# Optimization experiments

Hardware: AMD Instinct MI355X
Metric: run time of the kernel (lower is better)

## Reference

```python
import jax, jax.numpy as jnp
import numpy as np

ROPE_DIM = 64
ROPE_THETA = 10000.0
SLIDING_WINDOW = 1024
_K_MASK = jnp.finfo(jnp.bfloat16).min


def _pos_embeddings(positions, head_dim, rope_theta):
    # positions: [B, T] -> sin, cos: [B, T, head_dim]
    fraction = jnp.arange(0, head_dim, 2, dtype=jnp.float32) / head_dim
    inv_freq = 1.0 / (rope_theta ** fraction)
    sinusoid = jnp.einsum('BT,k->BTk', positions.astype(jnp.float32), inv_freq,
                          precision=jax.lax.Precision.HIGHEST)
    sin = jnp.sin(sinusoid); cos = jnp.cos(sinusoid)
    return jnp.concatenate([sin, sin], -1), jnp.concatenate([cos, cos], -1)


def _rotate_half(x):
    x1, x2 = x[..., :x.shape[-1] // 2], x[..., x.shape[-1] // 2:]
    return jnp.concatenate([-x2, x1], -1)


def _apply_rope_partial(x, sin, cos, rope_dim):
    x_rope, x_nope = x[..., :rope_dim], x[..., rope_dim:]
    sin = sin[:, :, None, :]; cos = cos[:, :, None, :]
    x_rope = x_rope * cos + _rotate_half(x_rope) * sin
    return jnp.concatenate([x_rope, x_nope], -1).astype(x.dtype)


def setup_inputs() -> dict:
    key = jax.random.key(0)
    ks = jax.random.split(key, 6)
    B, T, D = 2, 2048, 2048
    N, K, H, Hv = 16, 4, 128, 128
    S = 2048  # cache size
    sc = 0.02
    return {
        'x': jax.random.normal(ks[0], (B, T, D), jnp.float32),
        'wq': jax.random.normal(ks[1], (D, N, H), jnp.float32) * sc,
        'wk': jax.random.normal(ks[2], (D, K, H), jnp.float32) * sc,
        'wv': jax.random.normal(ks[3], (D, K, Hv), jnp.float32) * sc,
        'wo': jax.random.normal(ks[4], (N, Hv, D), jnp.float32) * sc,
        'sink_bias': jnp.zeros((N,), jnp.float32),
        'k_cache': jnp.zeros((B, S, K, H), jnp.float32),
        'v_cache': jnp.zeros((B, S, K, Hv), jnp.float32),
        'segment_ids': jnp.ones((B, T), jnp.int32),
        'cur_ind': 0,
        'start_ind': -jnp.ones((B,), jnp.int32),
    }


def reference(x, wq, wk, wv, wo, sink_bias, k_cache, v_cache,
              segment_ids, cur_ind, start_ind):
    B, T, D = x.shape
    N, H = wq.shape[1], wq.shape[2]
    K, Hv = wk.shape[1], wv.shape[2]
    n_rep = N // K
    scaling = H ** -0.5
    cur_ind = jnp.asarray(cur_ind, jnp.int32)

    q = jnp.einsum('BTD,DNH->BTNH', x, wq)
    k = jnp.einsum('BSD,DKH->BSKH', x, wk)
    v = jnp.einsum('BSD,DKV->BSKV', x, wv)

    # left pads / positions from segment ids
    left_pads = jnp.sum(jnp.cumsum(segment_ids != 0, axis=-1) == 0, -1).astype(jnp.int32)
    start = jnp.where(start_ind < 0, left_pads, start_ind)
    pos = jax.vmap(lambda row: jnp.where(row != 0,
                                         jnp.arange(T, dtype=jnp.int32) - jnp.argmax(row).astype(jnp.int32),
                                         2 ** 30))(segment_ids) + cur_ind
    sin, cos = _pos_embeddings(pos, ROPE_DIM, ROPE_THETA)
    q = _apply_rope_partial(q, sin, cos, ROPE_DIM)
    k = _apply_rope_partial(k, sin, cos, ROPE_DIM)

    # KV cache append
    kc = jax.lax.dynamic_update_slice(k_cache, k, (0, cur_ind, 0, 0))
    vc = jax.lax.dynamic_update_slice(v_cache, v, (0, cur_ind, 0, 0))
    S = kc.shape[1]

    # GQA repeat
    kr = jnp.repeat(kc[:, :, :, None, :], n_rep, axis=3).reshape(B, S, N, H)
    vr = jnp.repeat(vc[:, :, :, None, :], n_rep, axis=3).reshape(B, S, N, Hv)

    logits = jnp.einsum('BTNH,BSNH->BTNS', q, kr) * scaling

    q_pos = cur_ind + jnp.arange(T, dtype=jnp.int32)[None, :] - start[:, None]
    ts = jnp.arange(S, dtype=jnp.int32)
    kv_seg = (ts[None, :] >= start[:, None]) & (ts[None, :] < cur_ind + T)
    k_pos = ts[None, :] - start[:, None]
    causal = k_pos[:, None, :] <= q_pos[:, :, None]
    seg_mask = kv_seg[:, None, :] == segment_ids[:, :, None]
    window = k_pos[:, None, :] >= q_pos[:, :, None] - (SLIDING_WINDOW - 1)
    final_mask = causal & seg_mask & window  # [B, T, S]
    logits = jnp.where(final_mask[:, :, None, :], logits, _K_MASK)

    # attention sink bias: extra softmax slot per head
    sink = jnp.broadcast_to(sink_bias[None, None, :, None], (B, T, N, 1))
    logits = jnp.concatenate([logits, sink], axis=-1)
    weights = jax.nn.softmax(logits.astype(jnp.float32), axis=-1).astype(logits.dtype)
    weights = weights[..., :-1]

    attn = jnp.einsum('BTNS,BSNV->BTNV', weights, vr)
    return jnp.einsum('BTNV,NVD->BTD', attn, wo)
```

## Files before the change

### kernel.cpp

```cpp
#include <hip/hip_runtime.h>
#include <hip/hip_bf16.h>
#include <stdint.h>

#define BB 2
#define TT 2048
#define DD 2048
#define NHQ 16
#define KH 4
#define HD 128
#define SS 2048
#define WINDOW 1024
#define M2FIX 12.0f
#define QSC_LOG2E 0.12751751f
#define LOG2E 1.4426950408889634f
#define NLOG2F 0.4152410118609203f

typedef __attribute__((ext_vector_type(8))) short bf16x8;
typedef __attribute__((ext_vector_type(4))) float f32x4;
typedef __attribute__((ext_vector_type(16))) float f32x16;

#define MFMA16(a, b, c) __builtin_amdgcn_mfma_f32_16x16x32_bf16(a, b, c, 0, 0, 0)
#define MFMA32(a, b, c) __builtin_amdgcn_mfma_f32_32x32x16_bf16(a, b, c, 0, 0, 0)

__device__ __forceinline__ ushort f2bf(float f) {
  uint32_t u = __float_as_uint(f);
  u += 0x7FFF + ((u >> 16) & 1);
  return (ushort)(u >> 16);
}
__device__ __forceinline__ ushort f2bf_trunc(float f) {
  return (ushort)(__float_as_uint(f) >> 16);
}
__device__ __forceinline__ float bf2f(ushort h) {
  return __uint_as_float(((uint32_t)h) << 16);
}

__device__ __forceinline__ void async_copy16(const ushort* g, ushort* l) {
  __builtin_amdgcn_global_load_lds(
      (const __attribute__((address_space(1))) uint32_t*)g,
      (__attribute__((address_space(3))) uint32_t*)l, 16, 0, 0);
}

__device__ __forceinline__ void tr_tile(const float* __restrict__ in,
                                        ushort* __restrict__ out,
                                        int C, int ldo, int cx, int cy) {
  __shared__ float tile[32][33];
  int tx = threadIdx.x & 31, ty = threadIdx.x >> 5;
  int r0 = cy * 32, c0 = cx * 32;
#pragma unroll
  for (int k = 0; k < 4; k++)
    tile[ty + k * 8][tx] = in[(size_t)(r0 + ty + k * 8) * C + c0 + tx];
  __syncthreads();
#pragma unroll
  for (int k = 0; k < 4; k++)
    out[(size_t)(c0 + ty + k * 8) * ldo + r0 + tx] = f2bf(tile[tx][ty + k * 8]);
}

__global__ void prep_fused(const float* __restrict__ x, const float* __restrict__ wq,
                           const float* __restrict__ wk, const float* __restrict__ wv,
                           const float* __restrict__ wo, const int* __restrict__ seg,
                           const int* __restrict__ start_ind, ushort* __restrict__ xb,
                           ushort* __restrict__ WcatT, ushort* __restrict__ WoT,
                           int* __restrict__ meta) {
  int bz = blockIdx.x;
  int tid = threadIdx.x;
  if (bz < 2) {
    __shared__ int red[256];
    int b = bz;
    int first = TT;
    for (int t = tid; t < TT; t += 256)
      if (seg[b * TT + t] != 0) first = min(first, t);
    red[tid] = first;
    __syncthreads();
    for (int s = 128; s > 0; s >>= 1) {
      if (tid < s) red[tid] = min(red[tid], red[tid + s]);
      __syncthreads();
    }
    if (tid == 0) {
      int fi = red[0];
      int st = start_ind[b] < 0 ? fi : start_ind[b];
      meta[b * 2 + 0] = st;
      meta[b * 2 + 1] = (fi >= TT) ? 0 : fi;
    }
    return;
  }
  bz -= 2;
  if (bz < 2048) {
#pragma unroll
    for (int p = 0; p < 4; p++) {
      int i = bz * 1024 + p * 256 + tid;
      float4 v = ((const float4*)x)[i];
      ushort4 o;
      o.x = f2bf(v.x); o.y = f2bf(v.y); o.z = f2bf(v.z); o.w = f2bf(v.w);
      ((ushort4*)xb)[i] = o;
    }
    return;
  }
  bz -= 2048;
  if (bz < 4096) { tr_tile(wq, WcatT, 2048, 2048, bz & 63, bz >> 6); return; }
  bz -= 4096;
  if (bz < 1024) { tr_tile(wk, WcatT + (size_t)2048 * 2048, 512, 2048, bz & 15, bz >> 4); return; }
  bz -= 1024;
  if (bz < 1024) { tr_tile(wv, WcatT + (size_t)2560 * 2048, 512, 2048, bz & 15, bz >> 4); return; }
  bz -= 1024;
  tr_tile(wo, WoT, 2048, 2048, bz & 63, bz >> 6);
}

__global__ __launch_bounds__(256) void gemm_qkv(const ushort* __restrict__ A,
                                                const ushort* __restrict__ Bt,
                                                const int* __restrict__ seg,
                                                const int* __restrict__ cur_p,
                                                const int* __restrict__ meta,
                                                ushort* __restrict__ qa,
                                                ushort* __restrict__ ka,
                                                ushort* __restrict__ vat) {
  const int K = DD;
  __shared__ ushort SH[16640];
  ushort* As = SH;
  ushort* Bs = SH + 8192;
  float* posf_s = (float*)(SH + 16384);
  int tid = threadIdx.x;
  int lane = tid & 63, wave = tid >> 6;
  int wr = wave >> 1, wc = wave & 1;
  int orig = blockIdx.y * 24 + blockIdx.x;
  int wid = (orig & 7) * 96 + (orig >> 3);
  int by = wid / 24, bx = wid - by * 24;
  int row0 = by * 128, col0 = bx * 128;
  int l31 = lane & 31, khalf = lane >> 5, lx8 = l31 & 7;
  int cur = cur_p[0];

  if (tid < 128) {
    int m = row0 + tid;
    int bb = m >> 11, t = m & 2047;
    int segv = seg[m];
    int first = meta[bb * 2 + 1];
    posf_s[tid] = (segv != 0) ? (float)(t - first + cur) : 1073741824.0f;
  }

  f32x16 acc[2][2];
#pragma unroll
  for (int i = 0; i < 2; i++)
#pragma unroll
    for (int j = 0; j < 2; j++)
#pragma unroll
      for (int e = 0; e < 16; e++) acc[i][j][e] = 0.f;

  int srow = tid >> 3, scol = tid & 7;
  int ssw = (scol ^ (srow & 7)) * 8;
  const ushort* Ag = A  + (size_t)(row0 + srow) * K + ssw;
  const ushort* Bg = Bt + (size_t)(col0 + srow) * K + ssw;
  ushort* AsD = As + tid * 8;
  ushort* BsD = Bs + tid * 8;

  for (int kc = 0; kc < K; kc += 64) {
    __syncthreads();
#pragma unroll
    for (int p = 0; p < 4; p++)
      async_copy16(Ag + kc + (size_t)(p * 32) * K, AsD + p * 2048);
#pragma unroll
    for (int p = 0; p < 4; p++)
      async_copy16(Bg + kc + (size_t)(p * 32) * K, BsD + p * 2048);
    __syncthreads();
#pragma unroll
    for (int ks = 0; ks < 4; ks++) {
      bf16x8 af[2], bfm[2];
      int ch = (ks * 2 + khalf) ^ lx8;
#pragma unroll
      for (int i = 0; i < 2; i++)
        af[i] = *(const bf16x8*)(As + (wr * 64 + i * 32 + l31) * 64 + ch * 8);
#pragma unroll
      for (int j = 0; j < 2; j++)
        bfm[j] = *(const bf16x8*)(Bs + (wc * 64 + j * 32 + l31) * 64 + ch * 8);
#pragma unroll
      for (int i = 0; i < 2; i++)
#pragma unroll
        for (int j = 0; j < 2; j++)
          acc[i][j] = MFMA32(af[i], bfm[j], acc[i][j]);
    }
  }

  int cb0 = col0 + wc * 64;
  int region = (cb0 < 2048) ? 0 : (cb0 < 2560 ? 1 : 2);

  if (region <= 1) {
    bool ropehalf = ((cb0 & 64) == 0);
    int hbase = cb0 & 64;
    float invf = exp2f(-NLOG2F * (float)l31);
#pragma unroll
    for (int i = 0; i < 2; i++) {
#pragma unroll
      for (int reg = 0; reg < 16; reg++) {
        int rloc = wr * 64 + i * 32 + (reg & 3) + 8 * (reg >> 2) + 4 * khalf;
        int m = row0 + rloc;
        int b = m >> 11, t = m & 2047;
        float v0 = acc[i][0][reg], v1 = acc[i][1][reg];
        if (ropehalf) {
          float posf = posf_s[rloc];
          float sn, cs;
          __sincosf(posf * invf, &sn, &cs);
          float n0 = v0 * cs - v1 * sn;
          v1 = v1 * cs + v0 * sn;
          v0 = n0;
        }
        if (region == 0) {
          int head = cb0 >> 7;
          size_t base = ((size_t)(b * NHQ + head) * TT + t) * HD + hbase;
          qa[base + l31]      = f2bf(v0 * QSC_LOG2E);
          qa[base + 32 + l31] = f2bf(v1 * QSC_LOG2E);
        } else {
          int head = (cb0 - 2048) >> 7;
          size_t rowbase = ((size_t)(b * KH + head) * SS + t) * HD;
          int sw = t & 7;
          int c0x = hbase + l31, c1x = hbase + 32 + l31;
          ka[rowbase + ((((c0x >> 3) ^ sw) << 3) | (c0x & 7))] = f2bf(v0);
          ka[rowbase + ((((c1x >> 3) ^ sw) << 3) | (c1x & 7))] = f2bf(v1);
        }
      }
    }
  } else {
    __syncthreads();
    ushort* TB = SH;
    int hbase = wc * 64;
#pragma unroll
    for (int i = 0; i < 2; i++)
#pragma unroll
      for (int reg = 0; reg < 16; reg++) {
        int rloc = wr * 64 + i * 32 + (reg & 3) + 8 * (reg >> 2) + 4 * khalf;
        int h0 = hbase + l31, h1 = hbase + 32 + l31;
        TB[h0 * 128 + (rloc ^ ((h0 & 15) << 3))] = f2bf(acc[i][0][reg]);
        TB[h1 * 128 + (rloc ^ ((h1 & 15) << 3))] = f2bf(acc[i][1][reg]);
      }
    __syncthreads();
    int headv = (col0 - 2560) >> 7;
    int bv = row0 >> 11;
    ushort* vout = vat + (size_t)(bv * KH + headv) * HD * SS + (row0 & 2047);
#pragma unroll
    for (int pass = 0; pass < 8; pass++) {
      int idx = pass * 256 + tid;
      int h = idx >> 4, cc = idx & 15;
      int s64 = cc >> 3, c = cc & 7;
      bf16x8 vd = *(const bf16x8*)(TB + h * 128 + (s64 ^ ((h >> 3) & 1)) * 64 + c * 8);
      *(bf16x8*)(vout + (size_t)h * SS + s64 * 64 + c * 8) = vd;
    }
  }
}

template <int OUT_F32>
__global__ __launch_bounds__(256) void gemm_bt(const ushort* __restrict__ A,
                                               const ushort* __restrict__ Bt,
                                               void* __restrict__ Cout,
                                               int M, int N, int K) {
  __shared__ ushort As[128 * 64];
  __shared__ ushort Bs[128 * 64];
  int tid = threadIdx.x;
  int lane = tid & 63, wave = tid >> 6;
  int wr = wave >> 1, wc = wave & 1;
  int orig = blockIdx.y * gridDim.x + blockIdx.x;
  int nwg = gridDim.x * gridDim.y;
  int cpx = nwg >> 3;
  int wid = (orig & 7) * cpx + (orig >> 3);
  int by = wid / gridDim.x, bx = wid - by * gridDim.x;
  int row0 = by * 128, col0 = bx * 128;
  int l31 = lane & 31, khalf = lane >> 5, lx8 = l31 & 7;

  f32x16 acc[2][2];
#pragma unroll
  for (int i = 0; i < 2; i++)
#pragma unroll
    for (int j = 0; j < 2; j++)
#pragma unroll
      for (int e = 0; e < 16; e++) acc[i][j][e] = 0.f;

  int srow = tid >> 3, scol = tid & 7;
  int ssw = (scol ^ (srow & 7)) * 8;
  const ushort* Ag = A  + (size_t)(row0 + srow) * K + ssw;
  const ushort* Bg = Bt + (size_t)(col0 + srow) * K + ssw;
  ushort* AsD = As + tid * 8;
  ushort* BsD = Bs + tid * 8;

  for (int kc = 0; kc < K; kc += 64) {
    __syncthreads();
#pragma unroll
    for (int p = 0; p < 4; p++)
      async_copy16(Ag + kc + (size_t)(p * 32) * K, AsD + p * 2048);
#pragma unroll
    for (int p = 0; p < 4; p++)
      async_copy16(Bg + kc + (size_t)(p * 32) * K, BsD + p * 2048);
    __syncthreads();
#pragma unroll
    for (int ks = 0; ks < 4; ks++) {
      bf16x8 af[2], bfm[2];
      int ch = (ks * 2 + khalf) ^ lx8;
#pragma unroll
      for (int i = 0; i < 2; i++)
        af[i] = *(const bf16x8*)(As + (wr * 64 + i * 32 + l31) * 64 + ch * 8);
#pragma unroll
      for (int j = 0; j < 2; j++)
        bfm[j] = *(const bf16x8*)(Bs + (wc * 64 + j * 32 + l31) * 64 + ch * 8);
#pragma unroll
      for (int i = 0; i < 2; i++)
#pragma unroll
        for (int j = 0; j < 2; j++)
          acc[i][j] = MFMA32(af[i], bfm[j], acc[i][j]);
    }
  }

#pragma unroll
  for (int i = 0; i < 2; i++)
#pragma unroll
    for (int reg = 0; reg < 16; reg++) {
      int r = row0 + wr * 64 + i * 32 + (reg & 3) + 8 * (reg >> 2) + 4 * khalf;
#pragma unroll
      for (int j = 0; j < 2; j++) {
        int c = col0 + wc * 64 + j * 32 + l31;
        float v = acc[i][j][reg];
        if (OUT_F32)
          ((float*)Cout)[(size_t)r * N + c] = v;
        else
          ((ushort*)Cout)[(size_t)r * N + c] = f2bf(v);
      }
    }
}

__global__ __launch_bounds__(256) void flash_attn(
    const ushort* __restrict__ qa, const ushort* __restrict__ ka,
    const ushort* __restrict__ vat, const float* __restrict__ sink_bias,
    const int* __restrict__ seg, const int* __restrict__ cur_p,
    const int* __restrict__ meta, ushort* __restrict__ Obuf) {
  __shared__ ushort Ks[64 * 128];
  __shared__ ushort VT[128 * 64];
  __shared__ ushort Ps[4 * 2048];

  int bxx = blockIdx.x;
  int kb = bxx & 3, b = (bxx >> 2) & 1;
  int jr = bxx >> 3;
  int j32 = (jr & 1) ? (63 - (jr >> 1)) : (jr >> 1);
  int t0 = j32 * 32;
  int cur = cur_p[0];
  int start = meta[b * 2];

  int tid = threadIdx.x, lane = tid & 63, w = tid >> 6;
  int n = kb * 4 + w;
  int lcol = lane & 15, quad = lane >> 4, lx = lcol & 7;

  const ushort* qbase = qa + (size_t)(b * NHQ + n) * TT * HD;
  const ushort* kbase = ka + (size_t)(b * KH + kb) * SS * HD;
  const ushort* vtb   = vat + (size_t)(b * KH + kb) * HD * SS;

  bf16x8 qf[2][4];
  int segq[2][4], trow[2][4], seg1[2];
#pragma unroll
  for (int g = 0; g < 2; g++) {
    const ushort* qrow = qbase + (size_t)(t0 + g * 16 + lcol) * HD + quad * 8;
#pragma unroll
    for (int c = 0; c < 4; c++) qf[g][c] = *(const bf16x8*)(qrow + c * 32);
#pragma unroll
    for (int r = 0; r < 4; r++) {
      trow[g][r] = t0 + g * 16 + quad * 4 + r;
      segq[g][r] = seg[b * TT + trow[g][r]];
    }
    seg1[g] = __all(segq[g][0] == 1 && segq[g][1] == 1 &&
                    segq[g][2] == 1 && segq[g][3] == 1);
  }

  f32x4 oacc[2][8], lacc[2];
#pragma unroll
  for (int g = 0; g < 2; g++) {
#pragma unroll
    for (int ob = 0; ob < 8; ob++) { f32x4 z = {0.f, 0.f, 0.f, 0.f}; oacc[g][ob] = z; }
    f32x4 z = {0.f, 0.f, 0.f, 0.f}; lacc[g] = z;
  }

  bf16x8 ones;
#pragma unroll
  for (int e = 0; e < 8; e++) ones[e] = (short)0x3F80;

  ushort* KsD = Ks + tid * 8;
  ushort* VTD = VT + tid * 8;
  const ushort* KgT = kbase + tid * 8;
  const ushort* VgT = vtb + (size_t)(tid >> 3) * SS + (tid & 7) * 8;

  int lo = cur + t0 - (WINDOW - 1); if (lo < 0) lo = 0;
  int hi = cur + t0 + 31;           if (hi > SS - 1) hi = SS - 1;
  int ktlo = lo >> 6, kthi = hi >> 6;

  for (int kt = ktlo; kt <= kthi; kt++) {
    int ks0 = kt * 64;
    __syncthreads();
#pragma unroll
    for (int p = 0; p < 4; p++)
      async_copy16(KgT + (size_t)ks0 * 128 + p * 2048, KsD + p * 2048);
#pragma unroll
    for (int p = 0; p < 4; p++)
      async_copy16(VgT + ks0 + (size_t)p * 32 * SS, VTD + p * 2048);
    __syncthreads();

#pragma unroll
    for (int g = 0; g < 2; g++) {
      int t0g = t0 + g * 16;
      bool active = (ks0 <= cur + t0g + 15) && (ks0 + 63 >= cur + t0g - (WINDOW - 1));
      if (!active) continue;

      ushort* PsG = Ps + w * 2048 + g * 1024;
      f32x4 sacc[4];
#pragma unroll
      for (int cb = 0; cb < 4; cb++) { f32x4 z = {0.f, 0.f, 0.f, 0.f}; sacc[cb] = z; }
#pragma unroll
      for (int c = 0; c < 4; c++) {
#pragma unroll
        for (int cb = 0; cb < 4; cb++) {
          bf16x8 kf = *(const bf16x8*)(Ks + (cb * 16 + lcol) * 128 +
                                       (((c * 4 + quad) ^ lx)) * 8);
          sacc[cb] = MFMA16(qf[g][c], kf, sacc[cb]);
        }
      }

      bool fast = seg1[g] && (ks0 >= start) && (ks0 + 63 <= cur + t0g) &&
                  (ks0 >= cur + t0g + 15 - (WINDOW - 1));
      if (fast) {
#pragma unroll
        for (int r = 0; r < 4; r++) {
          int row = quad * 4 + r;
#pragma unroll
          for (int cb = 0; cb < 4; cb++) {
            float p = exp2f(sacc[cb][r] - M2FIX);
            PsG[row * 64 + (((cb * 2 + (lcol >> 3)) ^ (row & 7)) * 8) + lx] = f2bf_trunc(p);
          }
        }
      } else {
        int sidx[4], kvseg[4];
#pragma unroll
        for (int cb = 0; cb < 4; cb++) {
          sidx[cb] = ks0 + cb * 16 + lcol;
          kvseg[cb] = (sidx[cb] >= start && sidx[cb] < cur + TT) ? 1 : 0;
        }
#pragma unroll
        for (int r = 0; r < 4; r++) {
          int row = quad * 4 + r;
          int qp = (segq[g][r] != 0) ? (cur + trow[g][r]) : (1 << 29);
#pragma unroll
          for (int cb = 0; cb < 4; cb++) {
            bool ok = (sidx[cb] <= qp) && (sidx[cb] >= qp - (WINDOW - 1)) &&
                      (kvseg[cb] == segq[g][r]);
            float p = ok ? exp2f(sacc[cb][r] - M2FIX) : 0.f;
            PsG[row * 64 + (((cb * 2 + (lcol >> 3)) ^ (row & 7)) * 8) + lx] = f2bf_trunc(p);
          }
        }
      }

#pragma unroll
      for (int c2 = 0; c2 < 2; c2++) {
        bf16x8 pf = *(const bf16x8*)(PsG + lcol * 64 + (((c2 * 4 + quad) ^ lx)) * 8);
#pragma unroll
        for (int ob = 0; ob < 8; ob++) {
          bf16x8 vf = *(const bf16x8*)(VT + (ob * 16 + lcol) * 64 +
                                       (((c2 * 4 + quad) ^ lx)) * 8);
          oacc[g][ob] = MFMA16(pf, vf, oacc[g][ob]);
        }
        lacc[g] = MFMA16(pf, ones, lacc[g]);
      }
    }
  }

  float sb = sink_bias[n];
#pragma unroll
  for (int g = 0; g < 2; g++) {
#pragma unroll
    for (int r = 0; r < 4; r++) {
      float l = lacc[g][r] + exp2f(sb * LOG2E - M2FIX);
      float inv = 1.f / l;
      int t = trow[g][r];
      size_t base = ((size_t)(b * TT + t)) * (NHQ * HD) + n * HD;
#pragma unroll
      for (int ob = 0; ob < 8; ob++)
        Obuf[base + ob * 16 + lcol] = f2bf(oacc[g][ob][r] * inv);
    }
  }
}

extern "C" void kernel_launch(void* const* d_in, const int* in_sizes, int n_in,
                              void* d_out, int out_size, void* d_ws, size_t ws_size,
                              hipStream_t stream) {
  const float* x  = (const float*)d_in[0];
  const float* wq = (const float*)d_in[1];
  const float* wk = (const float*)d_in[2];
  const float* wv = (const float*)d_in[3];
  const float* wo = (const float*)d_in[4];
  const float* sink = (const float*)d_in[5];
  const int* seg = (const int*)d_in[8];
  const int* cur = (const int*)d_in[9];
  const int* start_ind = (const int*)d_in[10];

  char* ws = (char*)d_ws;
  ushort* xb    = (ushort*)(ws + 0);
  ushort* WcatT = (ushort*)(ws + 16777216);
  ushort* WoT   = (ushort*)(ws + 29360128);
  ushort* qa    = (ushort*)(ws + 37748736);
  ushort* ka    = (ushort*)(ws + 54525952);
  ushort* vat   = (ushort*)(ws + 62914560);
  ushort* Obuf  = (ushort*)(ws + 67108864);
  int*    meta  = (int*)(ws + 83886080);

  prep_fused<<<12290, 256, 0, stream>>>(x, wq, wk, wv, wo, seg, start_ind,
                                        xb, WcatT, WoT, meta);
  gemm_qkv<<<dim3(24, 32), 256, 0, stream>>>(xb, WcatT, seg, cur, meta, qa, ka, vat);
  flash_attn<<<512, 256, 0, stream>>>(qa, ka, vat, sink, seg, cur, meta, Obuf);
  gemm_bt<1><<<dim3(16, 32), 256, 0, stream>>>(Obuf, WoT, d_out, 4096, 2048, 2048);
}
```

Baseline: 333.7 us.

## Restructure flash attention to one head per block and vectorize transpose tiles

The attention kernel moves from blocks of four heads sharing a KV group over 32 query rows to blocks of two waves handling one head over 64 query rows, each wave covering 32 rows. The QK and PV MFMAs for both 16-row groups are interleaved so each K and V fragment read from LDS feeds two MFMAs, and the grid gets a new query-tile order meant to balance load. In exchange, each K/V tile load now serves one head instead of four, which increases KV traffic, and inactive groups write explicit zeros to Ps. The prep transpose tile is also changed to use float4 loads and ushort4 stores.

```diff
diff --git a/kernel.cpp b/kernel.cpp
--- a/kernel.cpp
+++ b/kernel.cpp
@@ -43,16 +43,20 @@
 __device__ __forceinline__ void tr_tile(const float* __restrict__ in,
                                         ushort* __restrict__ out,
                                         int C, int ldo, int cx, int cy) {
-  __shared__ float tile[32][33];
-  int tx = threadIdx.x & 31, ty = threadIdx.x >> 5;
+  __shared__ float tile[32][36];
+  int t = threadIdx.x;
   int r0 = cy * 32, c0 = cx * 32;
-#pragma unroll
-  for (int k = 0; k < 4; k++)
-    tile[ty + k * 8][tx] = in[(size_t)(r0 + ty + k * 8) * C + c0 + tx];
+  int row = t >> 3, c4 = (t & 7) * 4;
+  float4 v = *(const float4*)&in[(size_t)(r0 + row) * C + c0 + c4];
+  *(float4*)&tile[row][c4] = v;
   __syncthreads();
-#pragma unroll
-  for (int k = 0; k < 4; k++)
-    out[(size_t)(c0 + ty + k * 8) * ldo + r0 + tx] = f2bf(tile[tx][ty + k * 8]);
+  int oc = t >> 3, or4 = (t & 7) * 4;
+  ushort4 o;
+  o.x = f2bf(tile[or4 + 0][oc]);
+  o.y = f2bf(tile[or4 + 1][oc]);
+  o.z = f2bf(tile[or4 + 2][oc]);
+  o.w = f2bf(tile[or4 + 3][oc]);
+  *(ushort4*)&out[(size_t)(c0 + oc) * ldo + r0 + or4] = o;
 }
 
 __global__ void prep_fused(const float* __restrict__ x, const float* __restrict__ wq,
@@ -321,26 +325,28 @@
     }
 }
 
-__global__ __launch_bounds__(256) void flash_attn(
+__global__ __launch_bounds__(128) void flash_attn(
     const ushort* __restrict__ qa, const ushort* __restrict__ ka,
     const ushort* __restrict__ vat, const float* __restrict__ sink_bias,
     const int* __restrict__ seg, const int* __restrict__ cur_p,
     const int* __restrict__ meta, ushort* __restrict__ Obuf) {
   __shared__ ushort Ks[64 * 128];
   __shared__ ushort VT[128 * 64];
-  __shared__ ushort Ps[4 * 2048];
-
-  int bxx = blockIdx.x;
-  int kb = bxx & 3, b = (bxx >> 2) & 1;
-  int jr = bxx >> 3;
-  int j32 = (jr & 1) ? (63 - (jr >> 1)) : (jr >> 1);
-  int t0 = j32 * 32;
+  __shared__ ushort Ps[4096];
+
+  int bx = blockIdx.x;
+  int u = bx & 255, v = bx >> 8;
+  int combo = u & 31, j5 = u >> 5;
+  int b = combo >> 4, n = combo & 15;
+  int qt = (v == 0) ? j5 : (v == 1) ? (15 - j5) : (v == 2) ? (16 + j5) : (31 - j5);
+  int kb = n >> 2;
+  int t0 = qt * 64;
   int cur = cur_p[0];
   int start = meta[b * 2];
 
   int tid = threadIdx.x, lane = tid & 63, w = tid >> 6;
-  int n = kb * 4 + w;
   int lcol = lane & 15, quad = lane >> 4, lx = lcol & 7;
+  int tw = t0 + w * 32;
 
   const ushort* qbase = qa + (size_t)(b * NHQ + n) * TT * HD;
   const ushort* kbase = ka + (size_t)(b * KH + kb) * SS * HD;
@@ -350,12 +356,12 @@
   int segq[2][4], trow[2][4], seg1[2];
 #pragma unroll
   for (int g = 0; g < 2; g++) {
-    const ushort* qrow = qbase + (size_t)(t0 + g * 16 + lcol) * HD + quad * 8;
+    const ushort* qrow = qbase + (size_t)(tw + g * 16 + lcol) * HD + quad * 8;
 #pragma unroll
     for (int c = 0; c < 4; c++) qf[g][c] = *(const bf16x8*)(qrow + c * 32);
 #pragma unroll
     for (int r = 0; r < 4; r++) {
-      trow[g][r] = t0 + g * 16 + quad * 4 + r;
+      trow[g][r] = tw + g * 16 + quad * 4 + r;
       segq[g][r] = seg[b * TT + trow[g][r]];
     }
     seg1[g] = __all(segq[g][0] == 1 && segq[g][1] == 1 &&
@@ -370,9 +376,9 @@
     f32x4 z = {0.f, 0.f, 0.f, 0.f}; lacc[g] = z;
   }
 
-  bf16x8 ones;
-#pragma unroll
-  for (int e = 0; e < 8; e++) ones[e] = (short)0x3F80;
+  bf16x8 ones, zeros;
+#pragma unroll
+  for (int e = 0; e < 8; e++) { ones[e] = (short)0x3F80; zeros[e] = 0; }
 
   ushort* KsD = Ks + tid * 8;
   ushort* VTD = VT + tid * 8;
@@ -380,40 +386,52 @@
   const ushort* VgT = vtb + (size_t)(tid >> 3) * SS + (tid & 7) * 8;
 
   int lo = cur + t0 - (WINDOW - 1); if (lo < 0) lo = 0;
-  int hi = cur + t0 + 31;           if (hi > SS - 1) hi = SS - 1;
+  int hi = cur + t0 + 63;           if (hi > SS - 1) hi = SS - 1;
   int ktlo = lo >> 6, kthi = hi >> 6;
+
+  ushort* PsW = Ps + w * 2048;
 
   for (int kt = ktlo; kt <= kthi; kt++) {
     int ks0 = kt * 64;
     __syncthreads();
 #pragma unroll
-    for (int p = 0; p < 4; p++)
-      async_copy16(KgT + (size_t)ks0 * 128 + p * 2048, KsD + p * 2048);
-#pragma unroll
-    for (int p = 0; p < 4; p++)
-      async_copy16(VgT + ks0 + (size_t)p * 32 * SS, VTD + p * 2048);
-    __syncthreads();
+    for (int p = 0; p < 8; p++)
+      async_copy16(KgT + (size_t)ks0 * 128 + p * 1024, KsD + p * 1024);
+#pragma unroll
+    for (int p = 0; p < 8; p++)
+      async_copy16(VgT + ks0 + (size_t)p * 16 * SS, VTD + p * 1024);
+    __syncthreads();
+
+    int act0 = (ks0 <= cur + tw + 15)      && (ks0 + 63 >= cur + tw - (WINDOW - 1));
+    int act1 = (ks0 <= cur + tw + 16 + 15) && (ks0 + 63 >= cur + tw + 16 - (WINDOW - 1));
+    if (!(act0 | act1)) continue;
+
+    f32x4 sacc[2][4];
+#pragma unroll
+    for (int g = 0; g < 2; g++)
+#pragma unroll
+      for (int cb = 0; cb < 4; cb++) { f32x4 z = {0.f, 0.f, 0.f, 0.f}; sacc[g][cb] = z; }
+#pragma unroll
+    for (int c = 0; c < 4; c++) {
+#pragma unroll
+      for (int cb = 0; cb < 4; cb++) {
+        bf16x8 kf = *(const bf16x8*)(Ks + (cb * 16 + lcol) * 128 +
+                                     (((c * 4 + quad) ^ lx)) * 8);
+        sacc[0][cb] = MFMA16(qf[0][c], kf, sacc[0][cb]);
+        sacc[1][cb] = MFMA16(qf[1][c], kf, sacc[1][cb]);
+      }
+    }
 
 #pragma unroll
     for (int g = 0; g < 2; g++) {
-      int t0g = t0 + g * 16;
-      bool active = (ks0 <= cur + t0g + 15) && (ks0 + 63 >= cur + t0g - (WINDOW - 1));
-      if (!active) continue;
-
-      ushort* PsG = Ps + w * 2048 + g * 1024;
-      f32x4 sacc[4];
-#pragma unroll
-      for (int cb = 0; cb < 4; cb++) { f32x4 z = {0.f, 0.f, 0.f, 0.f}; sacc[cb] = z; }
-#pragma unroll
-      for (int c = 0; c < 4; c++) {
-#pragma unroll
-        for (int cb = 0; cb < 4; cb++) {
-          bf16x8 kf = *(const bf16x8*)(Ks + (cb * 16 + lcol) * 128 +
-                                       (((c * 4 + quad) ^ lx)) * 8);
-          sacc[cb] = MFMA16(qf[g][c], kf, sacc[cb]);
-        }
-      }
-
+      ushort* PsG = PsW + g * 1024;
+      int act = g ? act1 : act0;
+      if (!act) {
+        *(bf16x8*)(PsG + lane * 16) = zeros;
+        *(bf16x8*)(PsG + lane * 16 + 8) = zeros;
+        continue;
+      }
+      int t0g = tw + g * 16;
       bool fast = seg1[g] && (ks0 >= start) && (ks0 + 63 <= cur + t0g) &&
                   (ks0 >= cur + t0g + 15 - (WINDOW - 1));
       if (fast) {
@@ -422,7 +440,7 @@
           int row = quad * 4 + r;
 #pragma unroll
           for (int cb = 0; cb < 4; cb++) {
-            float p = exp2f(sacc[cb][r] - M2FIX);
+            float p = exp2f(sacc[g][cb][r] - M2FIX);
             PsG[row * 64 + (((cb * 2 + (lcol >> 3)) ^ (row & 7)) * 8) + lx] = f2bf_trunc(p);
           }
         }
@@ -441,23 +459,26 @@
           for (int cb = 0; cb < 4; cb++) {
             bool ok = (sidx[cb] <= qp) && (sidx[cb] >= qp - (WINDOW - 1)) &&
                       (kvseg[cb] == segq[g][r]);
-            float p = ok ? exp2f(sacc[cb][r] - M2FIX) : 0.f;
+            float p = ok ? exp2f(sacc[g][cb][r] - M2FIX) : 0.f;
             PsG[row * 64 + (((cb * 2 + (lcol >> 3)) ^ (row & 7)) * 8) + lx] = f2bf_trunc(p);
           }
         }
       }
-
-#pragma unroll
-      for (int c2 = 0; c2 < 2; c2++) {
-        bf16x8 pf = *(const bf16x8*)(PsG + lcol * 64 + (((c2 * 4 + quad) ^ lx)) * 8);
-#pragma unroll
-        for (int ob = 0; ob < 8; ob++) {
-          bf16x8 vf = *(const bf16x8*)(VT + (ob * 16 + lcol) * 64 +
-                                       (((c2 * 4 + quad) ^ lx)) * 8);
-          oacc[g][ob] = MFMA16(pf, vf, oacc[g][ob]);
-        }
-        lacc[g] = MFMA16(pf, ones, lacc[g]);
-      }
+    }
+
+#pragma unroll
+    for (int c2 = 0; c2 < 2; c2++) {
+      bf16x8 pf0 = *(const bf16x8*)(PsW + lcol * 64 + (((c2 * 4 + quad) ^ lx)) * 8);
+      bf16x8 pf1 = *(const bf16x8*)(PsW + 1024 + lcol * 64 + (((c2 * 4 + quad) ^ lx)) * 8);
+#pragma unroll
+      for (int ob = 0; ob < 8; ob++) {
+        bf16x8 vf = *(const bf16x8*)(VT + (ob * 16 + lcol) * 64 +
+                                     (((c2 * 4 + quad) ^ lx)) * 8);
+        oacc[0][ob] = MFMA16(pf0, vf, oacc[0][ob]);
+        oacc[1][ob] = MFMA16(pf1, vf, oacc[1][ob]);
+      }
+      lacc[0] = MFMA16(pf0, ones, lacc[0]);
+      lacc[1] = MFMA16(pf1, ones, lacc[1]);
     }
   }
 
@@ -503,6 +524,6 @@
   prep_fused<<<12290, 256, 0, stream>>>(x, wq, wk, wv, wo, seg, start_ind,
                                         xb, WcatT, WoT, meta);
   gemm_qkv<<<dim3(24, 32), 256, 0, stream>>>(xb, WcatT, seg, cur, meta, qa, ka, vat);
-  flash_attn<<<512, 256, 0, stream>>>(qa, ka, vat, sink, seg, cur, meta, Obuf);
+  flash_attn<<<1024, 128, 0, stream>>>(qa, ka, vat, sink, seg, cur, meta, Obuf);
   gemm_bt<1><<<dim3(16, 32), 256, 0, stream>>>(Obuf, WoT, d_out, 4096, 2048, 2048);
 }
```

Result: no change. 331.4 us (-0.7%).
